# Performance work log

Measured on AMD Instinct MI355X. Metric: run time of the kernel, lower is better.

The kernel has to match this reference:

```python
import jax, jax.numpy as jnp
import numpy as np
from jax import lax

B, C, H, W_DIM = 32, 10, 128, 128  # C fixed at 10 by the module
K = 5


def setup_inputs() -> dict:
    key = jax.random.key(0)
    k1, k2, k3 = jax.random.split(key, 3)
    x = jax.random.normal(k1, (B, C, H, W_DIM), dtype=jnp.float32)
    # Conv3d(in_channels=10, out_channels=10, kernel_size=5) weights, OIDHW layout
    fan_in = C * K * K * K
    bound = 1.0 / np.sqrt(fan_in)
    W = jax.random.uniform(k2, (C, C, K, K, K), dtype=jnp.float32, minval=-bound, maxval=bound)
    b = jax.random.uniform(k3, (C,), dtype=jnp.float32, minval=-bound, maxval=bound)
    return {"x": x, "W": W, "b": b}


def reference(x, W, b):
    # Original loop: t[idx] = x * mask(idx) zeroes every channel except idx;
    # stack(t, dim=1) is therefore a diagonal embed along a new depth axis.
    eye = jnp.eye(C, dtype=x.dtype)  # [D=10, C=10]
    stack_x = x[:, None, :, :, :] * eye[None, :, :, None, None]  # [B, 10, 10, H, W]
    out = lax.conv_general_dilated(
        stack_x, W,
        window_strides=(1, 1, 1),
        padding=((2, 2), (2, 2), (2, 2)),
        dimension_numbers=("NCDHW", "OIDHW", "NCDHW"),
    )
    return out + b[None, :, None, None, None]
```

## Files before the change

### kernel.cpp

```cpp
#include <hip/hip_runtime.h>


#define TILE_ROWS 8
#define LDS_ROWS  12
#define LDS_W     132
#define BLOCK     256

__global__ __launch_bounds__(BLOCK, 4)
void conv3d_diag_kernel(const float* __restrict__ x,
                        const float* __restrict__ Wt,
                        const float* __restrict__ bias,
                        float* __restrict__ out)
{
    __shared__ float lds[LDS_ROWS * LDS_W];

    const int tid  = threadIdx.x;
    const int tile = blockIdx.x;
    const int z    = blockIdx.y;
    const int n    = blockIdx.z;

    const int y0 = tile * TILE_ROWS;
    const int tx = tid & 31;
    const int ty = tid >> 5;
    const int x0 = tx << 2;
    const int y  = y0 + ty;

    float acc[10][4];
    #pragma unroll
    for (int o = 0; o < 10; ++o)
        #pragma unroll
        for (int p = 0; p < 4; ++p) acc[o][p] = 0.f;

    const float* xn = x + (size_t)n * (10 * 128 * 128);

    #pragma unroll 1
    for (int kd = 0; kd < 5; ++kd) {
        const int d = z + kd - 2;
        if (d < 0 || d >= 10) continue;
        const float* xp = xn + d * (128 * 128);

        __syncthreads();
        for (int e = tid; e < LDS_ROWS * LDS_W; e += BLOCK) {
            const int r  = e / LDS_W;
            const int c  = e - r * LDS_W;
            const int gr = y0 - 2 + r;
            const int gc = c - 2;
            float v = 0.f;
            if ((unsigned)gr < 128u && (unsigned)gc < 128u)
                v = xp[gr * 128 + gc];
            lds[e] = v;
        }
        __syncthreads();

        #pragma unroll 1
        for (int kh = 0; kh < 5; ++kh) {
            const float* wp = Wt + (size_t)(d * 125 + kd * 25 + kh * 5);
            float wv[10][5];
            #pragma unroll
            for (int o = 0; o < 10; ++o)
                #pragma unroll
                for (int kw = 0; kw < 5; ++kw)
                    wv[o][kw] = wp[o * 1250 + kw];

            const float* lp = &lds[(ty + kh) * LDS_W + x0];
            const float4 rlo = *(const float4*)(lp);
            const float4 rhi = *(const float4*)(lp + 4);
            const float r[8] = {rlo.x, rlo.y, rlo.z, rlo.w,
                                rhi.x, rhi.y, rhi.z, rhi.w};

            #pragma unroll
            for (int kw = 0; kw < 5; ++kw)
                #pragma unroll
                for (int o = 0; o < 10; ++o)
                    #pragma unroll
                    for (int p = 0; p < 4; ++p)
                        acc[o][p] += r[p + kw] * wv[o][kw];
        }
    }

    #pragma unroll
    for (int o = 0; o < 10; ++o) {
        const float bo = bias[o];
        const float4 v = make_float4(acc[o][0] + bo, acc[o][1] + bo,
                                     acc[o][2] + bo, acc[o][3] + bo);
        const size_t idx = ((((size_t)n * 10 + o) * 10 + z) * 128 + y) * 128 + x0;
        *(float4*)(out + idx) = v;
    }
}

extern "C" void kernel_launch(void* const* d_in, const int* in_sizes, int n_in,
                              void* d_out, int out_size, void* d_ws, size_t ws_size,
                              hipStream_t stream) {
    const float* x    = (const float*)d_in[0];
    const float* Wt   = (const float*)d_in[1];
    const float* bias = (const float*)d_in[2];
    float* out = (float*)d_out;

    dim3 grid(16, 10, 32);
    conv3d_diag_kernel<<<grid, BLOCK, 0, stream>>>(x, Wt, bias, out);
}
```

Baseline: 306.7 us.

## Compute two depth outputs per block with double-buffered async LDS plane loads

Each block now computes two consecutive output depth slices, so each input plane loaded into LDS feeds both slices' accumulators and the grid halves along depth. Plane loads use global_load_lds (direct global-to-LDS) into a double buffer with precomputed per-thread offsets, so the next plane's fetch overlaps compute on the current one. Weights are read inline per (o,kw) rather than staged in a register array. The cost is doubled accumulator registers (80 floats), which risks spills or lower occupancy under the 4-blocks launch bound, and half as many blocks.

```diff
diff --git a/kernel.cpp b/kernel.cpp
--- a/kernel.cpp
+++ b/kernel.cpp
@@ -4,7 +4,12 @@
 #define TILE_ROWS 8
 #define LDS_ROWS  12
 #define LDS_W     132
+#define PLANE_W   (LDS_ROWS * LDS_W)
 #define BLOCK     256
+#define NSLOT     7
+
+typedef const __attribute__((address_space(1))) void gvoid_t;
+typedef __attribute__((address_space(3))) void lvoid_t;
 
 __global__ __launch_bounds__(BLOCK, 4)
 void conv3d_diag_kernel(const float* __restrict__ x,
@@ -12,11 +17,11 @@
                         const float* __restrict__ bias,
                         float* __restrict__ out)
 {
-    __shared__ float lds[LDS_ROWS * LDS_W];
+    __shared__ float lds[2 * PLANE_W];
 
     const int tid  = threadIdx.x;
     const int tile = blockIdx.x;
-    const int z    = blockIdx.y;
+    const int z0   = blockIdx.y << 1;
     const int n    = blockIdx.z;
 
     const int y0 = tile * TILE_ROWS;
@@ -25,66 +30,118 @@
     const int x0 = tx << 2;
     const int y  = y0 + ty;
 
-    float acc[10][4];
+    int goff[NSLOT];
     #pragma unroll
-    for (int o = 0; o < 10; ++o)
+    for (int s = 0; s < NSLOT; ++s) {
+        const int e  = tid + s * BLOCK;
+        const int r  = e / LDS_W;
+        const int c  = e - r * LDS_W;
+        const int gr = y0 - 2 + r;
+        const int gc = c - 2;
+        const bool ok = (e < PLANE_W) && ((unsigned)gr < 128u) && ((unsigned)gc < 128u);
+        goff[s] = ok ? (gr * 128 + gc) : -1;
+    }
+    const int lbase = tid & ~63;
+
+    for (int e = tid; e < 2 * PLANE_W; e += BLOCK) lds[e] = 0.f;
+
+    float acc[2][10][4];
+    #pragma unroll
+    for (int zi = 0; zi < 2; ++zi)
         #pragma unroll
-        for (int p = 0; p < 4; ++p) acc[o][p] = 0.f;
+        for (int o = 0; o < 10; ++o)
+            #pragma unroll
+            for (int p = 0; p < 4; ++p) acc[zi][o][p] = 0.f;
 
     const float* xn = x + (size_t)n * (10 * 128 * 128);
+    const int d_lo = (z0 >= 2) ? z0 - 2 : 0;
+    const int d_hi = (z0 + 3 <= 9) ? z0 + 3 : 9;
 
+    __syncthreads();
+
+    {
+        const float* xp = xn + d_lo * (128 * 128);
+        #pragma unroll
+        for (int s = 0; s < NSLOT; ++s)
+            if (goff[s] >= 0)
+                __builtin_amdgcn_global_load_lds((gvoid_t*)(xp + goff[s]),
+                                                 (lvoid_t*)(lds + s * BLOCK + lbase),
+                                                 4, 0, 0);
+    }
+    __syncthreads();
+
+    int cur = 0;
     #pragma unroll 1
-    for (int kd = 0; kd < 5; ++kd) {
-        const int d = z + kd - 2;
-        if (d < 0 || d >= 10) continue;
-        const float* xp = xn + d * (128 * 128);
+    for (int d = d_lo; d <= d_hi; ++d) {
+        if (d < d_hi) {
+            const float* xp = xn + (d + 1) * (128 * 128);
+            float* nb = lds + (cur ^ 1) * PLANE_W;
+            #pragma unroll
+            for (int s = 0; s < NSLOT; ++s)
+                if (goff[s] >= 0)
+                    __builtin_amdgcn_global_load_lds((gvoid_t*)(xp + goff[s]),
+                                                     (lvoid_t*)(nb + s * BLOCK + lbase),
+                                                     4, 0, 0);
+        }
 
-        __syncthreads();
-        for (int e = tid; e < LDS_ROWS * LDS_W; e += BLOCK) {
-            const int r  = e / LDS_W;
-            const int c  = e - r * LDS_W;
-            const int gr = y0 - 2 + r;
-            const int gc = c - 2;
-            float v = 0.f;
-            if ((unsigned)gr < 128u && (unsigned)gc < 128u)
-                v = xp[gr * 128 + gc];
-            lds[e] = v;
-        }
-        __syncthreads();
+        const float* bc  = lds + cur * PLANE_W;
+        const int  kd0 = d - z0 + 2;
+        const int  kd1 = kd0 - 1;
+        const bool do0 = (unsigned)kd0 < 5u;
+        const bool do1 = (unsigned)kd1 < 5u;
+        const float* wd = Wt + d * 125;
 
-        #pragma unroll 1
+        #pragma unroll
         for (int kh = 0; kh < 5; ++kh) {
-            const float* wp = Wt + (size_t)(d * 125 + kd * 25 + kh * 5);
-            float wv[10][5];
-            #pragma unroll
-            for (int o = 0; o < 10; ++o)
-                #pragma unroll
-                for (int kw = 0; kw < 5; ++kw)
-                    wv[o][kw] = wp[o * 1250 + kw];
-
-            const float* lp = &lds[(ty + kh) * LDS_W + x0];
+            const float* lp = bc + (ty + kh) * LDS_W + x0;
             const float4 rlo = *(const float4*)(lp);
             const float4 rhi = *(const float4*)(lp + 4);
             const float r[8] = {rlo.x, rlo.y, rlo.z, rlo.w,
                                 rhi.x, rhi.y, rhi.z, rhi.w};
 
-            #pragma unroll
-            for (int kw = 0; kw < 5; ++kw)
+            if (do0) {
+                const float* wp = wd + kd0 * 25 + kh * 5;
                 #pragma unroll
-                for (int o = 0; o < 10; ++o)
+                for (int kw = 0; kw < 5; ++kw)
                     #pragma unroll
-                    for (int p = 0; p < 4; ++p)
-                        acc[o][p] += r[p + kw] * wv[o][kw];
+                    for (int o = 0; o < 10; ++o) {
+                        const float wv = wp[o * 1250 + kw];
+                        #pragma unroll
+                        for (int p = 0; p < 4; ++p)
+                            acc[0][o][p] += r[p + kw] * wv;
+                    }
+            }
+            if (do1) {
+                const float* wp = wd + kd1 * 25 + kh * 5;
+                #pragma unroll
+                for (int kw = 0; kw < 5; ++kw)
+                    #pragma unroll
+                    for (int o = 0; o < 10; ++o) {
+                        const float wv = wp[o * 1250 + kw];
+                        #pragma unroll
+                        for (int p = 0; p < 4; ++p)
+                            acc[1][o][p] += r[p + kw] * wv;
+                    }
+            }
+        }
+
+        if (d < d_hi) {
+            __syncthreads();
+            cur ^= 1;
         }
     }
 
     #pragma unroll
-    for (int o = 0; o < 10; ++o) {
-        const float bo = bias[o];
-        const float4 v = make_float4(acc[o][0] + bo, acc[o][1] + bo,
-                                     acc[o][2] + bo, acc[o][3] + bo);
-        const size_t idx = ((((size_t)n * 10 + o) * 10 + z) * 128 + y) * 128 + x0;
-        *(float4*)(out + idx) = v;
+    for (int zi = 0; zi < 2; ++zi) {
+        const int z = z0 + zi;
+        #pragma unroll
+        for (int o = 0; o < 10; ++o) {
+            const float bo = bias[o];
+            const float4 v = make_float4(acc[zi][o][0] + bo, acc[zi][o][1] + bo,
+                                         acc[zi][o][2] + bo, acc[zi][o][3] + bo);
+            const size_t idx = ((((size_t)n * 10 + o) * 10 + z) * 128 + y) * 128 + x0;
+            *(float4*)(out + idx) = v;
+        }
     }
 }
 
@@ -96,6 +153,6 @@
     const float* bias = (const float*)d_in[2];
     float* out = (float*)d_out;
 
-    dim3 grid(16, 10, 32);
+    dim3 grid(16, 5, 32);
     conv3d_diag_kernel<<<grid, BLOCK, 0, stream>>>(x, Wt, bias, out);
 }
```

Result: slower. 555.8 us (+81.2%).
